# Kernel optimization log

Hardware: AMD Instinct MI355X
Metric: run time of the kernel (lower is better)

The kernel has to match this reference:

```python
import jax, jax.numpy as jnp
import numpy as np

NU = 0.01 / np.pi  # viscosity buffer from the torch module


def _mlp(x, W_in, b_in, W_hid, b_hid, W_out, b_out):
    # x: [N, 2] -> u: [N, 1]; tanh MLP with stacked hidden layers scanned.
    h = jnp.tanh(x @ W_in + b_in)

    def step(h, wb):
        W, b = wb
        return jnp.tanh(h @ W + b), None

    h, _ = jax.lax.scan(step, h, (W_hid, b_hid))
    return h @ W_out + b_out


def setup_inputs() -> dict:
    key = jax.random.key(0)
    ks = jax.random.split(key, 10)
    N_f, N0, Nb, H, L = 131072, 4096, 2048, 128, 7
    s_in = 1.0 / np.sqrt(2.0)
    s_h = 1.0 / np.sqrt(H)
    return {
        "x_f": jax.random.normal(ks[0], (N_f, 2), jnp.float32),
        "x0_cat": jax.random.normal(ks[1], (N0, 2), jnp.float32),
        "xb_left_cat": jax.random.normal(ks[2], (Nb, 2), jnp.float32),
        "xb_right_cat": jax.random.normal(ks[3], (Nb, 2), jnp.float32),
        "W_in": jax.random.normal(ks[4], (2, H), jnp.float32) * s_in,
        "b_in": jax.random.normal(ks[5], (H,), jnp.float32) * 0.01,
        "W_hid": jax.random.normal(ks[6], (L, H, H), jnp.float32) * s_h,
        "b_hid": jax.random.normal(ks[7], (L, H), jnp.float32) * 0.01,
        "W_out": jax.random.normal(ks[8], (H, 1), jnp.float32) * s_h,
        "b_out": jax.random.normal(ks[9], (1,), jnp.float32) * 0.01,
    }


def reference(x_f, x0_cat, xb_left_cat, xb_right_cat,
              W_in, b_in, W_hid, b_hid, W_out, b_out):
    u = lambda x: _mlp(x, W_in, b_in, W_hid, b_hid, W_out, b_out)

    u_0_pred = u(x0_cat)
    u_b_left_pred = u(xb_left_cat)
    u_b_right_pred = u(xb_right_cat)

    u_f_pred = u(x_f)  # [N_f, 1]

    # Each row of u depends only on the matching row of x, so grad of the sum
    # yields per-example gradients (equivalent to torch.autograd.grad with
    # grad_outputs=ones).
    usum = lambda x: u(x).sum()
    g = jax.grad(usum)(x_f)            # [N_f, 2]
    u_x = g[:, 0:1]
    u_t = g[:, 1:2]

    # Second derivative: grad of sum(u_x) w.r.t. x, take the x-component.
    uxx_full = jax.grad(lambda x: jax.grad(usum)(x)[:, 0].sum())(x_f)
    u_xx = uxx_full[:, 0:1]

    pde_residual = u_t + u_f_pred * u_x - NU * u_xx
    return jnp.concatenate((u_0_pred, u_b_left_pred, u_b_right_pred,
                            pde_residual), axis=0)
```

## Files before the change

### kernel.cpp

```cpp
#include <hip/hip_runtime.h>
#include <math.h>

#define NU_F 0.0031830988618379067f
#define KTANH 2.885390082f

typedef _Float16 f16x8 __attribute__((ext_vector_type(8)));
typedef float    f32x4 __attribute__((ext_vector_type(4)));

__device__ __forceinline__ float tanh_pre(float zs) {
    float e = __builtin_amdgcn_exp2f(zs);
    float r = __builtin_amdgcn_rcpf(e + 1.0f);
    return fmaf(-2.0f, r, 1.0f);
}

__device__ __forceinline__ unsigned pkf16(float a, float b) {
    auto v = __builtin_amdgcn_cvt_pkrtz(a, b);
    return __builtin_bit_cast(unsigned, v);
}

__device__ __forceinline__ void lds_barrier() {
    asm volatile("s_waitcnt lgkmcnt(0)" ::: "memory");
    __builtin_amdgcn_s_barrier();
}

__global__ void prep_wfrag(const float* __restrict__ Whid, _Float16* __restrict__ wcf)
{
    const int t    = blockIdx.x * 256 + threadIdx.x;
    const int lane = t & 63;
    const int fid  = t >> 6;
    const int ks = fid & 3;
    const int nt = (fid >> 2) & 7;
    const int l  = fid >> 5;
    const int q  = lane >> 4;
    const int nn = lane & 15;
    const int c  = ((nt >> 1) << 5) + nn * 2 + (nt & 1);
    const int k0 = ks * 32 + q * 8;
    const float* src = Whid + l * 16384 + k0 * 128 + c;
    f16x8 v;
    #pragma unroll
    for (int jj = 0; jj < 8; ++jj)
        v[jj] = (_Float16)src[jj * 128];
    *(f16x8*)(wcf + (size_t)t * 8) = v;
}

#define HR 68
#define MFMA(A, B, C) __builtin_amdgcn_mfma_f32_16x16x32_f16((A), (B), (C), 0, 0, 0)

__device__ __forceinline__ void kloop(f32x4 (&acc)[4][2],
        const unsigned* __restrict__ Hc,
        const f16x8& cB0, const f16x8& cB1,
        const _Float16* __restrict__ pb0, const _Float16* __restrict__ pb1,
        int lm, int lq)
{
    #pragma unroll
    for (int s = 0; s < 4; ++s)
        #pragma unroll
        for (int j = 0; j < 2; ++j) acc[s][j] = (f32x4){0.f, 0.f, 0.f, 0.f};
    {
        const int ro = lq * 4;
        const f16x8 ah0 = *(const f16x8*)&Hc[(0 * 16 + lm) * HR + ro];
        const f16x8 ah1 = *(const f16x8*)&Hc[(1 * 16 + lm) * HR + ro];
        const f16x8 ah2 = *(const f16x8*)&Hc[(2 * 16 + lm) * HR + ro];
        const f16x8 ah3 = *(const f16x8*)&Hc[(3 * 16 + lm) * HR + ro];
        acc[0][0] = MFMA(ah0, cB0, acc[0][0]);
        acc[1][0] = MFMA(ah1, cB0, acc[1][0]);
        acc[2][0] = MFMA(ah2, cB0, acc[2][0]);
        acc[3][0] = MFMA(ah3, cB0, acc[3][0]);
        acc[0][1] = MFMA(ah0, cB1, acc[0][1]);
        acc[1][1] = MFMA(ah1, cB1, acc[1][1]);
        acc[2][1] = MFMA(ah2, cB1, acc[2][1]);
        acc[3][1] = MFMA(ah3, cB1, acc[3][1]);
    }
    #pragma unroll
    for (int ks = 1; ks < 4; ++ks) {
        const int ro = ks * 16 + lq * 4;
        const f16x8 ah0 = *(const f16x8*)&Hc[(0 * 16 + lm) * HR + ro];
        const f16x8 ah1 = *(const f16x8*)&Hc[(1 * 16 + lm) * HR + ro];
        const f16x8 ah2 = *(const f16x8*)&Hc[(2 * 16 + lm) * HR + ro];
        const f16x8 ah3 = *(const f16x8*)&Hc[(3 * 16 + lm) * HR + ro];
        const f16x8 b0 = *(const f16x8*)(pb0 + ks * 512);
        const f16x8 b1 = *(const f16x8*)(pb1 + ks * 512);
        acc[0][0] = MFMA(ah0, b0, acc[0][0]);
        acc[1][0] = MFMA(ah1, b0, acc[1][0]);
        acc[2][0] = MFMA(ah2, b0, acc[2][0]);
        acc[3][0] = MFMA(ah3, b0, acc[3][0]);
        acc[0][1] = MFMA(ah0, b1, acc[0][1]);
        acc[1][1] = MFMA(ah1, b1, acc[1][1]);
        acc[2][1] = MFMA(ah2, b1, acc[2][1]);
        acc[3][1] = MFMA(ah3, b1, acc[3][1]);
    }
}

__device__ __forceinline__ void epi_deriv(const f32x4 (&acc)[4][2],
        float bbs0, float bbs1, unsigned* __restrict__ Hn, int lq, int wc)
{
    #pragma unroll
    for (int r = 0; r < 4; ++r) {
        const int p = lq * 4 + r;
        float h[2][4];
        #pragma unroll
        for (int j = 0; j < 2; ++j) {
            const float zx  = acc[1][j][r];
            const float zt  = acc[2][j][r];
            const float zxx = acc[3][j][r];
            const float y = tanh_pre(fmaf(acc[0][j][r], KTANH, j ? bbs1 : bbs0));
            const float d = fmaf(-y, y, 1.f);
            const float m = d * zx;
            h[j][0] = y;
            h[j][1] = m;
            h[j][2] = d * zt;
            h[j][3] = fmaf(d, zxx, -2.f * (y * m) * zx);
        }
        #pragma unroll
        for (int s = 0; s < 4; ++s)
            Hn[(s * 16 + p) * HR + wc] = pkf16(h[0][s], h[1][s]);
    }
}

__device__ __forceinline__ void epi_val(const f32x4 (&acc)[4][2],
        float bbs0, float bbs1, unsigned* __restrict__ Hn, int lq, int wc)
{
    #pragma unroll
    for (int mt = 0; mt < 4; ++mt) {
        #pragma unroll
        for (int r = 0; r < 4; ++r) {
            const int p = mt * 16 + lq * 4 + r;
            const float y0 = tanh_pre(fmaf(acc[mt][0][r], KTANH, bbs0));
            const float y1 = tanh_pre(fmaf(acc[mt][1][r], KTANH, bbs1));
            Hn[p * HR + wc] = pkf16(y0, y1);
        }
    }
}

__global__ __launch_bounds__(256, 4)
void pinn_fused(const float* __restrict__ xf,
                const float* __restrict__ x0,  const float* __restrict__ xbl,
                const float* __restrict__ xbr,
                const float* __restrict__ Win,  const float* __restrict__ bin,
                const float* __restrict__ bhid,
                const float* __restrict__ Wout, const float* __restrict__ bout,
                const _Float16* __restrict__ wcf,
                float* __restrict__ out)
{
    __shared__ unsigned Hh[2][64 * HR];
    __shared__ float xpt[256];
    __shared__ float pbuf[512];
    __shared__ float dots[128];

    const int tid  = threadIdx.x;
    const int lane = tid & 63;
    const int wv   = tid >> 6;
    const int lm   = lane & 15;
    const int lq   = lane >> 4;
    const int blk  = blockIdx.x;
    const bool isv = (blk >= 4096);

    if (!isv) {
        if (tid < 64) xpt[tid] = xf[blk * 64 + tid];
    } else {
        const int vb = blk - 4096;
        const int vp = vb * 2 + (tid >> 7);
        const float* src = (vp < 64) ? (x0 + vp * 128)
                         : (vp < 96) ? (xbl + (vp - 64) * 128)
                                     : (xbr + (vp - 96) * 128);
        xpt[tid] = src[tid & 127];
    }

    const _Float16* pb0 = wcf + (wv * 2 + 0) * 2048 + lane * 8;
    const _Float16* pb1 = wcf + (wv * 2 + 1) * 2048 + lane * 8;
    const float* bptr = bhid + wv * 32 + lm * 2;
    f16x8 cB0 = *(const f16x8*)pb0;
    f16x8 cB1 = *(const f16x8*)pb1;
    float2 btc_cur = *(const float2*)bptr;
    float2 btc_prev;

    __syncthreads();

    const int cp = tid & 63;
    {
        const float2 w01 = *(const float2*)&Win[cp * 2];
        const float2 w11 = *(const float2*)&Win[128 + cp * 2];
        const float2 bb  = *(const float2*)&bin[cp * 2];
        const float w01sx = w01.x * KTANH, w01sy = w01.y * KTANH;
        const float w11sx = w11.x * KTANH, w11sy = w11.y * KTANH;
        const float bbsx  = bb.x  * KTANH, bbsy  = bb.y  * KTANH;
        if (!isv) {
            #pragma unroll
            for (int g = 0; g < 2; ++g) {
                const int xo = g * 32;
                const int p0 = wv * 4;
                #pragma unroll
                for (int i = 0; i < 4; ++i) {
                    const int p = p0 + i;
                    const float x = xpt[xo + 2 * p], tt = xpt[xo + 2 * p + 1];
                    const float ya = tanh_pre(fmaf(x, w01sx, fmaf(tt, w11sx, bbsx)));
                    const float yb = tanh_pre(fmaf(x, w01sy, fmaf(tt, w11sy, bbsy)));
                    const float da = 1.f - ya * ya, db = 1.f - yb * yb;
                    unsigned* H = Hh[g];
                    H[(0 * 16 + p) * HR + cp] = pkf16(ya, yb);
                    H[(1 * 16 + p) * HR + cp] = pkf16(da * w01.x, db * w01.y);
                    H[(2 * 16 + p) * HR + cp] = pkf16(da * w11.x, db * w11.y);
                    H[(3 * 16 + p) * HR + cp] =
                        pkf16(-2.f * ya * da * w01.x * w01.x,
                              -2.f * yb * db * w01.y * w01.y);
                }
            }
        } else {
            #pragma unroll
            for (int g = 0; g < 2; ++g) {
                const int xo = g * 128;
                const int p0 = wv * 16;
                #pragma unroll
                for (int i = 0; i < 16; ++i) {
                    const int p = p0 + i;
                    const float x = xpt[xo + 2 * p], tt = xpt[xo + 2 * p + 1];
                    const float ya = tanh_pre(fmaf(x, w01sx, fmaf(tt, w11sx, bbsx)));
                    const float yb = tanh_pre(fmaf(x, w01sy, fmaf(tt, w11sy, bbsy)));
                    Hh[g][p * HR + cp] = pkf16(ya, yb);
                }
            }
        }
    }
    lds_barrier();

    const int wc = wv * 16 + lm;

    f32x4 accA[4][2], accB[4][2];

    if (!isv) {
        for (int l = 0; l < 7; ++l) {
            kloop(accA, Hh[0], cB0, cB1, pb0, pb1, lm, lq);
            if (l > 0)
                epi_deriv(accB, btc_prev.x * KTANH, btc_prev.y * KTANH,
                          Hh[1], lq, wc);
            lds_barrier();

            kloop(accB, Hh[1], cB0, cB1, pb0, pb1, lm, lq);
            btc_prev = btc_cur;
            pb0 += 16384; pb1 += 16384;
            if (l < 6) {
                cB0 = *(const f16x8*)pb0;
                cB1 = *(const f16x8*)pb1;
                btc_cur = *(const float2*)(bptr + 128);
                bptr += 128;
            }
            epi_deriv(accA, btc_prev.x * KTANH, btc_prev.y * KTANH,
                      Hh[0], lq, wc);
            lds_barrier();
        }
        epi_deriv(accB, btc_prev.x * KTANH, btc_prev.y * KTANH, Hh[1], lq, wc);
        lds_barrier();
    } else {
        for (int l = 0; l < 7; ++l) {
            kloop(accA, Hh[0], cB0, cB1, pb0, pb1, lm, lq);
            if (l > 0)
                epi_val(accB, btc_prev.x * KTANH, btc_prev.y * KTANH,
                        Hh[1], lq, wc);
            lds_barrier();

            kloop(accB, Hh[1], cB0, cB1, pb0, pb1, lm, lq);
            btc_prev = btc_cur;
            pb0 += 16384; pb1 += 16384;
            if (l < 6) {
                cB0 = *(const f16x8*)pb0;
                cB1 = *(const f16x8*)pb1;
                btc_cur = *(const float2*)(bptr + 128);
                bptr += 128;
            }
            epi_val(accA, btc_prev.x * KTANH, btc_prev.y * KTANH, Hh[0], lq, wc);
            lds_barrier();
        }
        epi_val(accB, btc_prev.x * KTANH, btc_prev.y * KTANH, Hh[1], lq, wc);
        lds_barrier();
    }

    {
        const int st = lane;
        const int cb = wv * 16;
        float pA = 0.f, pB = 0.f;
        #pragma unroll
        for (int c8 = 0; c8 < 4; ++c8) {
            const f16x8 hA = *(const f16x8*)&Hh[0][st * HR + cb + c8 * 4];
            const f16x8 hB = *(const f16x8*)&Hh[1][st * HR + cb + c8 * 4];
            const float4 w1 = *(const float4*)&Wout[wv * 32 + c8 * 8];
            const float4 w2 = *(const float4*)&Wout[wv * 32 + c8 * 8 + 4];
            pA = fmaf((float)hA[0], w1.x, pA);
            pA = fmaf((float)hA[1], w1.y, pA);
            pA = fmaf((float)hA[2], w1.z, pA);
            pA = fmaf((float)hA[3], w1.w, pA);
            pA = fmaf((float)hA[4], w2.x, pA);
            pA = fmaf((float)hA[5], w2.y, pA);
            pA = fmaf((float)hA[6], w2.z, pA);
            pA = fmaf((float)hA[7], w2.w, pA);
            pB = fmaf((float)hB[0], w1.x, pB);
            pB = fmaf((float)hB[1], w1.y, pB);
            pB = fmaf((float)hB[2], w1.z, pB);
            pB = fmaf((float)hB[3], w1.w, pB);
            pB = fmaf((float)hB[4], w2.x, pB);
            pB = fmaf((float)hB[5], w2.y, pB);
            pB = fmaf((float)hB[6], w2.z, pB);
            pB = fmaf((float)hB[7], w2.w, pB);
        }
        pbuf[wv * 64 + st] = pA;
        pbuf[256 + wv * 64 + st] = pB;
    }
    lds_barrier();
    if (tid < 128) {
        const float* q = pbuf + (tid >> 6) * 256;
        const int t = tid & 63;
        dots[tid] = (q[t] + q[64 + t]) + (q[128 + t] + q[192 + t]);
    }
    lds_barrier();
    if (!isv) {
        if (tid < 16) {
            const float u = dots[tid] + bout[0];
            out[8192 + blk * 32 + tid] =
                dots[32 + tid] + u * dots[16 + tid] - NU_F * dots[48 + tid];
        } else if (tid >= 64 && tid < 80) {
            const int t = tid - 64;
            const float u = dots[64 + t] + bout[0];
            out[8192 + blk * 32 + 16 + t] =
                dots[96 + t] + u * dots[80 + t] - NU_F * dots[112 + t];
        }
    } else {
        const int vb = blk - 4096;
        if (tid < 128)
            out[vb * 128 + tid] = dots[tid] + bout[0];
    }
}

extern "C" void kernel_launch(void* const* d_in, const int* in_sizes, int n_in,
                              void* d_out, int out_size, void* d_ws, size_t ws_size,
                              hipStream_t stream) {
    (void)in_sizes; (void)n_in; (void)ws_size; (void)out_size;
    const float* xf   = (const float*)d_in[0];
    const float* x0   = (const float*)d_in[1];
    const float* xbl  = (const float*)d_in[2];
    const float* xbr  = (const float*)d_in[3];
    const float* Win  = (const float*)d_in[4];
    const float* bin  = (const float*)d_in[5];
    const float* Whid = (const float*)d_in[6];
    const float* bhid = (const float*)d_in[7];
    const float* Wout = (const float*)d_in[8];
    const float* bout = (const float*)d_in[9];
    float* out = (float*)d_out;

    _Float16* wcf = (_Float16*)d_ws;

    hipLaunchKernelGGL(prep_wfrag, dim3(14336 / 256), dim3(256), 0, stream,
                       Whid, wcf);
    hipLaunchKernelGGL(pinn_fused, dim3(4096 + 64), dim3(256), 0, stream,
                       xf, x0, xbl, xbr, Win, bin, bhid, Wout, bout, wcf, out);
}
```

Before: 227.9 us.

## Split waves across the two point groups with 64-column tiles, dropping ping-pong overlap

Each wave now owns one of the two point groups and half of the 128 output columns, computing a 4x4 MFMA tile instead of all four waves sweeping both groups with 16x2 tiles in a software-pipelined ping-pong. The weight fragment layout is regrouped to four-column interleaving so each lane writes packed uint2 stores. This halves the A-fragment LDS reads per MFMA and the number of kloop calls per layer. In exchange it loses the overlap of one group's epilogue with the other group's matmul, adds a barrier per layer, and raises register pressure (launch bounds drop to 3 blocks per CU).

New measurement: 241.5 us. +6.0%, slower.

```diff
diff --git a/kernel.cpp b/kernel.cpp
--- a/kernel.cpp
+++ b/kernel.cpp
@@ -33,7 +33,7 @@
     const int l  = fid >> 5;
     const int q  = lane >> 4;
     const int nn = lane & 15;
-    const int c  = ((nt >> 1) << 5) + nn * 2 + (nt & 1);
+    const int c  = ((nt >> 2) << 6) + nn * 4 + (nt & 3);
     const int k0 = ks * 32 + q * 8;
     const float* src = Whid + l * 16384 + k0 * 128 + c;
     f16x8 v;
@@ -46,64 +46,75 @@
 #define HR 68
 #define MFMA(A, B, C) __builtin_amdgcn_mfma_f32_16x16x32_f16((A), (B), (C), 0, 0, 0)
 
-__device__ __forceinline__ void kloop(f32x4 (&acc)[4][2],
+__device__ __forceinline__ void kloop44(f32x4 (&acc)[4][4],
         const unsigned* __restrict__ Hc,
-        const f16x8& cB0, const f16x8& cB1,
-        const _Float16* __restrict__ pb0, const _Float16* __restrict__ pb1,
+        const f16x8 (&cB)[4],
+        const _Float16* __restrict__ pbase,
         int lm, int lq)
 {
     #pragma unroll
-    for (int s = 0; s < 4; ++s)
-        #pragma unroll
-        for (int j = 0; j < 2; ++j) acc[s][j] = (f32x4){0.f, 0.f, 0.f, 0.f};
+    for (int t = 0; t < 4; ++t)
+        #pragma unroll
+        for (int j = 0; j < 4; ++j) acc[t][j] = (f32x4){0.f, 0.f, 0.f, 0.f};
+
     {
         const int ro = lq * 4;
-        const f16x8 ah0 = *(const f16x8*)&Hc[(0 * 16 + lm) * HR + ro];
-        const f16x8 ah1 = *(const f16x8*)&Hc[(1 * 16 + lm) * HR + ro];
-        const f16x8 ah2 = *(const f16x8*)&Hc[(2 * 16 + lm) * HR + ro];
-        const f16x8 ah3 = *(const f16x8*)&Hc[(3 * 16 + lm) * HR + ro];
-        acc[0][0] = MFMA(ah0, cB0, acc[0][0]);
-        acc[1][0] = MFMA(ah1, cB0, acc[1][0]);
-        acc[2][0] = MFMA(ah2, cB0, acc[2][0]);
-        acc[3][0] = MFMA(ah3, cB0, acc[3][0]);
-        acc[0][1] = MFMA(ah0, cB1, acc[0][1]);
-        acc[1][1] = MFMA(ah1, cB1, acc[1][1]);
-        acc[2][1] = MFMA(ah2, cB1, acc[2][1]);
-        acc[3][1] = MFMA(ah3, cB1, acc[3][1]);
+        const f16x8 a0 = *(const f16x8*)&Hc[(0 * 16 + lm) * HR + ro];
+        const f16x8 a1 = *(const f16x8*)&Hc[(1 * 16 + lm) * HR + ro];
+        const f16x8 a2 = *(const f16x8*)&Hc[(2 * 16 + lm) * HR + ro];
+        const f16x8 a3 = *(const f16x8*)&Hc[(3 * 16 + lm) * HR + ro];
+        #pragma unroll
+        for (int j = 0; j < 4; ++j) {
+            acc[0][j] = MFMA(a0, cB[j], acc[0][j]);
+            acc[1][j] = MFMA(a1, cB[j], acc[1][j]);
+            acc[2][j] = MFMA(a2, cB[j], acc[2][j]);
+            acc[3][j] = MFMA(a3, cB[j], acc[3][j]);
+        }
     }
     #pragma unroll
     for (int ks = 1; ks < 4; ++ks) {
         const int ro = ks * 16 + lq * 4;
-        const f16x8 ah0 = *(const f16x8*)&Hc[(0 * 16 + lm) * HR + ro];
-        const f16x8 ah1 = *(const f16x8*)&Hc[(1 * 16 + lm) * HR + ro];
-        const f16x8 ah2 = *(const f16x8*)&Hc[(2 * 16 + lm) * HR + ro];
-        const f16x8 ah3 = *(const f16x8*)&Hc[(3 * 16 + lm) * HR + ro];
-        const f16x8 b0 = *(const f16x8*)(pb0 + ks * 512);
-        const f16x8 b1 = *(const f16x8*)(pb1 + ks * 512);
-        acc[0][0] = MFMA(ah0, b0, acc[0][0]);
-        acc[1][0] = MFMA(ah1, b0, acc[1][0]);
-        acc[2][0] = MFMA(ah2, b0, acc[2][0]);
-        acc[3][0] = MFMA(ah3, b0, acc[3][0]);
-        acc[0][1] = MFMA(ah0, b1, acc[0][1]);
-        acc[1][1] = MFMA(ah1, b1, acc[1][1]);
-        acc[2][1] = MFMA(ah2, b1, acc[2][1]);
-        acc[3][1] = MFMA(ah3, b1, acc[3][1]);
-    }
-}
-
-__device__ __forceinline__ void epi_deriv(const f32x4 (&acc)[4][2],
-        float bbs0, float bbs1, unsigned* __restrict__ Hn, int lq, int wc)
-{
+        const f16x8 a0 = *(const f16x8*)&Hc[(0 * 16 + lm) * HR + ro];
+        const f16x8 a1 = *(const f16x8*)&Hc[(1 * 16 + lm) * HR + ro];
+        const f16x8 a2 = *(const f16x8*)&Hc[(2 * 16 + lm) * HR + ro];
+        const f16x8 a3 = *(const f16x8*)&Hc[(3 * 16 + lm) * HR + ro];
+        const f16x8 b0 = *(const f16x8*)(pbase + 0 * 2048 + ks * 512);
+        const f16x8 b1 = *(const f16x8*)(pbase + 1 * 2048 + ks * 512);
+        const f16x8 b2 = *(const f16x8*)(pbase + 2 * 2048 + ks * 512);
+        const f16x8 b3 = *(const f16x8*)(pbase + 3 * 2048 + ks * 512);
+        acc[0][0] = MFMA(a0, b0, acc[0][0]);
+        acc[1][0] = MFMA(a1, b0, acc[1][0]);
+        acc[2][0] = MFMA(a2, b0, acc[2][0]);
+        acc[3][0] = MFMA(a3, b0, acc[3][0]);
+        acc[0][1] = MFMA(a0, b1, acc[0][1]);
+        acc[1][1] = MFMA(a1, b1, acc[1][1]);
+        acc[2][1] = MFMA(a2, b1, acc[2][1]);
+        acc[3][1] = MFMA(a3, b1, acc[3][1]);
+        acc[0][2] = MFMA(a0, b2, acc[0][2]);
+        acc[1][2] = MFMA(a1, b2, acc[1][2]);
+        acc[2][2] = MFMA(a2, b2, acc[2][2]);
+        acc[3][2] = MFMA(a3, b2, acc[3][2]);
+        acc[0][3] = MFMA(a0, b3, acc[0][3]);
+        acc[1][3] = MFMA(a1, b3, acc[1][3]);
+        acc[2][3] = MFMA(a2, b3, acc[2][3]);
+        acc[3][3] = MFMA(a3, b3, acc[3][3]);
+    }
+}
+
+__device__ __forceinline__ void epi_deriv4(const f32x4 (&acc)[4][4],
+        const float4 bt, unsigned* __restrict__ Hn, int lq, int wc)
+{
+    const float bbs[4] = {bt.x * KTANH, bt.y * KTANH, bt.z * KTANH, bt.w * KTANH};
     #pragma unroll
     for (int r = 0; r < 4; ++r) {
         const int p = lq * 4 + r;
-        float h[2][4];
-        #pragma unroll
-        for (int j = 0; j < 2; ++j) {
+        float h[4][4];
+        #pragma unroll
+        for (int j = 0; j < 4; ++j) {
             const float zx  = acc[1][j][r];
             const float zt  = acc[2][j][r];
             const float zxx = acc[3][j][r];
-            const float y = tanh_pre(fmaf(acc[0][j][r], KTANH, j ? bbs1 : bbs0));
+            const float y = tanh_pre(fmaf(acc[0][j][r], KTANH, bbs[j]));
             const float d = fmaf(-y, y, 1.f);
             const float m = d * zx;
             h[j][0] = y;
@@ -112,27 +123,37 @@
             h[j][3] = fmaf(d, zxx, -2.f * (y * m) * zx);
         }
         #pragma unroll
-        for (int s = 0; s < 4; ++s)
-            Hn[(s * 16 + p) * HR + wc] = pkf16(h[0][s], h[1][s]);
-    }
-}
-
-__device__ __forceinline__ void epi_val(const f32x4 (&acc)[4][2],
-        float bbs0, float bbs1, unsigned* __restrict__ Hn, int lq, int wc)
-{
+        for (int s = 0; s < 4; ++s) {
+            uint2 w;
+            w.x = pkf16(h[0][s], h[1][s]);
+            w.y = pkf16(h[2][s], h[3][s]);
+            *(uint2*)&Hn[(s * 16 + p) * HR + wc] = w;
+        }
+    }
+}
+
+__device__ __forceinline__ void epi_val4(const f32x4 (&acc)[4][4],
+        const float4 bt, unsigned* __restrict__ Hn, int lq, int wc)
+{
+    const float bbs[4] = {bt.x * KTANH, bt.y * KTANH, bt.z * KTANH, bt.w * KTANH};
     #pragma unroll
     for (int mt = 0; mt < 4; ++mt) {
         #pragma unroll
         for (int r = 0; r < 4; ++r) {
             const int p = mt * 16 + lq * 4 + r;
-            const float y0 = tanh_pre(fmaf(acc[mt][0][r], KTANH, bbs0));
-            const float y1 = tanh_pre(fmaf(acc[mt][1][r], KTANH, bbs1));
-            Hn[p * HR + wc] = pkf16(y0, y1);
-        }
-    }
-}
-
-__global__ __launch_bounds__(256, 4)
+            float y[4];
+            #pragma unroll
+            for (int j = 0; j < 4; ++j)
+                y[j] = tanh_pre(fmaf(acc[mt][j][r], KTANH, bbs[j]));
+            uint2 w;
+            w.x = pkf16(y[0], y[1]);
+            w.y = pkf16(y[2], y[3]);
+            *(uint2*)&Hn[p * HR + wc] = w;
+        }
+    }
+}
+
+__global__ __launch_bounds__(256, 3)
 void pinn_fused(const float* __restrict__ xf,
                 const float* __restrict__ x0,  const float* __restrict__ xbl,
                 const float* __restrict__ xbr,
@@ -150,6 +171,8 @@
     const int tid  = threadIdx.x;
     const int lane = tid & 63;
     const int wv   = tid >> 6;
+    const int g    = wv >> 1;
+    const int nh   = wv & 1;
     const int lm   = lane & 15;
     const int lq   = lane >> 4;
     const int blk  = blockIdx.x;
@@ -166,13 +189,12 @@
         xpt[tid] = src[tid & 127];
     }
 
-    const _Float16* pb0 = wcf + (wv * 2 + 0) * 2048 + lane * 8;
-    const _Float16* pb1 = wcf + (wv * 2 + 1) * 2048 + lane * 8;
-    const float* bptr = bhid + wv * 32 + lm * 2;
-    f16x8 cB0 = *(const f16x8*)pb0;
-    f16x8 cB1 = *(const f16x8*)pb1;
-    float2 btc_cur = *(const float2*)bptr;
-    float2 btc_prev;
+    const _Float16* pbase = wcf + nh * 8192 + lane * 8;
+    const float* bptr = bhid + nh * 64 + lm * 4;
+    f16x8 cB[4];
+    #pragma unroll
+    for (int j = 0; j < 4; ++j) cB[j] = *(const f16x8*)(pbase + j * 2048);
+    float4 btc = *(const float4*)bptr;
 
     __syncthreads();
 
@@ -186,8 +208,8 @@
         const float bbsx  = bb.x  * KTANH, bbsy  = bb.y  * KTANH;
         if (!isv) {
             #pragma unroll
-            for (int g = 0; g < 2; ++g) {
-                const int xo = g * 32;
+            for (int gg = 0; gg < 2; ++gg) {
+                const int xo = gg * 32;
                 const int p0 = wv * 4;
                 #pragma unroll
                 for (int i = 0; i < 4; ++i) {
@@ -196,7 +218,7 @@
                     const float ya = tanh_pre(fmaf(x, w01sx, fmaf(tt, w11sx, bbsx)));
                     const float yb = tanh_pre(fmaf(x, w01sy, fmaf(tt, w11sy, bbsy)));
                     const float da = 1.f - ya * ya, db = 1.f - yb * yb;
-                    unsigned* H = Hh[g];
+                    unsigned* H = Hh[gg];
                     H[(0 * 16 + p) * HR + cp] = pkf16(ya, yb);
                     H[(1 * 16 + p) * HR + cp] = pkf16(da * w01.x, db * w01.y);
                     H[(2 * 16 + p) * HR + cp] = pkf16(da * w11.x, db * w11.y);
@@ -207,8 +229,8 @@
             }
         } else {
             #pragma unroll
-            for (int g = 0; g < 2; ++g) {
-                const int xo = g * 128;
+            for (int gg = 0; gg < 2; ++gg) {
+                const int xo = gg * 128;
                 const int p0 = wv * 16;
                 #pragma unroll
                 for (int i = 0; i < 16; ++i) {
@@ -216,62 +238,49 @@
                     const float x = xpt[xo + 2 * p], tt = xpt[xo + 2 * p + 1];
                     const float ya = tanh_pre(fmaf(x, w01sx, fmaf(tt, w11sx, bbsx)));
                     const float yb = tanh_pre(fmaf(x, w01sy, fmaf(tt, w11sy, bbsy)));
-                    Hh[g][p * HR + cp] = pkf16(ya, yb);
+                    Hh[gg][p * HR + cp] = pkf16(ya, yb);
                 }
             }
         }
     }
     lds_barrier();
 
-    const int wc = wv * 16 + lm;
-
-    f32x4 accA[4][2], accB[4][2];
+    const int wc = nh * 32 + lm * 2;
+    unsigned* Hg = Hh[g];
+    f32x4 acc[4][4];
 
     if (!isv) {
         for (int l = 0; l < 7; ++l) {
-            kloop(accA, Hh[0], cB0, cB1, pb0, pb1, lm, lq);
-            if (l > 0)
-                epi_deriv(accB, btc_prev.x * KTANH, btc_prev.y * KTANH,
-                          Hh[1], lq, wc);
-            lds_barrier();
-
-            kloop(accB, Hh[1], cB0, cB1, pb0, pb1, lm, lq);
-            btc_prev = btc_cur;
-            pb0 += 16384; pb1 += 16384;
+            kloop44(acc, Hg, cB, pbase, lm, lq);
+            const float4 bt = btc;
+            pbase += 16384;
             if (l < 6) {
-                cB0 = *(const f16x8*)pb0;
-                cB1 = *(const f16x8*)pb1;
-                btc_cur = *(const float2*)(bptr + 128);
+                #pragma unroll
+                for (int j = 0; j < 4; ++j)
+                    cB[j] = *(const f16x8*)(pbase + j * 2048);
+                btc = *(const float4*)(bptr + 128);
                 bptr += 128;
             }
-            epi_deriv(accA, btc_prev.x * KTANH, btc_prev.y * KTANH,
-                      Hh[0], lq, wc);
             lds_barrier();
-        }
-        epi_deriv(accB, btc_prev.x * KTANH, btc_prev.y * KTANH, Hh[1], lq, wc);
-        lds_barrier();
+            epi_deriv4(acc, bt, Hg, lq, wc);
+            lds_barrier();
+        }
     } else {
         for (int l = 0; l < 7; ++l) {
-            kloop(accA, Hh[0], cB0, cB1, pb0, pb1, lm, lq);
-            if (l > 0)
-                epi_val(accB, btc_prev.x * KTANH, btc_prev.y * KTANH,
-                        Hh[1], lq, wc);
-            lds_barrier();
-
-            kloop(accB, Hh[1], cB0, cB1, pb0, pb1, lm, lq);
-            btc_prev = btc_cur;
-            pb0 += 16384; pb1 += 16384;
+            kloop44(acc, Hg, cB, pbase, lm, lq);
+            const float4 bt = btc;
+            pbase += 16384;
             if (l < 6) {
-                cB0 = *(const f16x8*)pb0;
-                cB1 = *(const f16x8*)pb1;
-                btc_cur = *(const float2*)(bptr + 128);
+                #pragma unroll
+                for (int j = 0; j < 4; ++j)
+                    cB[j] = *(const f16x8*)(pbase + j * 2048);
+                btc = *(const float4*)(bptr + 128);
                 bptr += 128;
             }
-            epi_val(accA, btc_prev.x * KTANH, btc_prev.y * KTANH, Hh[0], lq, wc);
             lds_barrier();
-        }
-        epi_val(accB, btc_prev.x * KTANH, btc_prev.y * KTANH, Hh[1], lq, wc);
-        lds_barrier();
+            epi_val4(acc, bt, Hg, lq, wc);
+            lds_barrier();
+        }
     }
 
     {
```
